# Performance work log

Measured on AMD Instinct MI355X. Metric: run time of the kernel, lower is better.

The kernel has to match this reference:

```python
import jax, jax.numpy as jnp
import numpy as np

B, C, L = 16, 256, 2048

def setup_inputs() -> dict:
    key = jax.random.key(0)
    y = jax.random.normal(key, (B, C, L), dtype=jnp.float32)
    alpha = jnp.float32(0.5)
    beta = jnp.float32(0.5)
    gamma = jnp.float32(0.0)
    return {"y": y, "alpha": alpha, "beta": beta, "gamma": gamma}

def reference(y, alpha, beta, gamma):
    # y: [B, C, L]
    Bs, Cs, Ls = y.shape
    # channel attention: scores over channels, scaled by 1/sqrt(L)
    scale_c = 1.0 / np.sqrt(max(Ls, 1)).astype(np.float32)
    scores_c = jnp.einsum('bcl,bdl->bcd', y, y) * scale_c          # [B, C, C]
    attn_c = jax.nn.softmax(scores_c, axis=-1)
    y_c = jnp.einsum('bcd,bdl->bcl', attn_c, y)                    # [B, C, L]
    # time attention: scores over time steps, scaled by 1/sqrt(C)
    scale_t = 1.0 / np.sqrt(max(Cs, 1)).astype(np.float32)
    scores_t = jnp.einsum('bcl,bcm->blm', y, y) * scale_t          # [B, L, L]
    attn_t = jax.nn.softmax(scores_t, axis=-1)
    y_t = jnp.einsum('blm,bcm->bcl', attn_t, y)                    # [B, C, L]
    # learnable weighted combine + residual (gamma)
    out = alpha * y_c + beta * y_t + gamma * y
    return out
```

## Files before the change

### kernel.cpp

```cpp
#include <hip/hip_runtime.h>

#define B_ 16
#define C_ 256
#define L_ 2048

typedef __attribute__((ext_vector_type(8))) short short8;
typedef __attribute__((ext_vector_type(4))) float float4v;

__device__ inline float4v mfma16(short8 a, short8 b, float4v c) {
  return __builtin_amdgcn_mfma_f32_16x16x32_bf16(a, b, c, 0, 0, 0);
}

__device__ inline ushort f2bf(float x) {
  union { float f; unsigned u; } v; v.f = x;
  unsigned r = (v.u + 0x7fffu + ((v.u >> 16) & 1u)) >> 16;
  return (ushort)r;
}

__device__ inline void dma16(const ushort* g, void* l) {
  __builtin_amdgcn_global_load_lds(
      (const __attribute__((address_space(1))) unsigned int*)(g),
      (__attribute__((address_space(3))) unsigned int*)(l), 16, 0, 0);
}

#define BAR_FULL() asm volatile("s_waitcnt vmcnt(0) lgkmcnt(0)\ns_barrier" ::: "memory")
#define BAR_LGKM() asm volatile("s_waitcnt lgkmcnt(0)\ns_barrier" ::: "memory")

__global__ __launch_bounds__(256) void cvt_kernel(const float* __restrict__ y,
                                                  ushort* __restrict__ yb,
                                                  ushort* __restrict__ ytb) {
  __shared__ float tile[32][33];
  int b = blockIdx.z, ct = blockIdx.y, lt = blockIdx.x;
  int tx = threadIdx.x & 31, ty = threadIdx.x >> 5;
  size_t base = ((size_t)b * C_ + (size_t)ct * 32) * L_ + (size_t)lt * 32;
#pragma unroll
  for (int i = 0; i < 4; ++i) {
    int r = ty + i * 8;
    float v = y[base + (size_t)r * L_ + tx];
    tile[r][tx] = v;
    yb[base + (size_t)r * L_ + tx] = f2bf(v);
  }
  __syncthreads();
  size_t tbase = ((size_t)b * L_ + (size_t)lt * 32) * C_ + (size_t)ct * 32;
#pragma unroll
  for (int i = 0; i < 4; ++i) {
    int r = ty + i * 8;
    ytb[tbase + (size_t)r * C_ + tx] = f2bf(tile[tx][r]);
  }
}

__global__ __launch_bounds__(256) void chan_kernel(
    const ushort* __restrict__ yb, const ushort* __restrict__ ytb,
    const float* __restrict__ y, float* __restrict__ out,
    const float* __restrict__ alpha_p, const float* __restrict__ gamma_p) {
  const int blk = blockIdx.x;
  const int b = (blk & 7) + 8 * ((blk >> 3) & 1);
  const int rest = blk >> 4;
  const int m0 = (rest & 15) * 16;
  const int Lh = rest >> 4;
  const int tid = threadIdx.x;
  const int w = tid >> 6, lane = tid & 63, quad = lane >> 4, l16 = lane & 15;
  const float scale = 0.022097086912079608f;
  const float SHIFT = 45.0f;

  __shared__ __align__(16) unsigned char Tb[2][32768];
  __shared__ ushort Pl[16 * 264];
  __shared__ float wsum[4][16];
  __shared__ float ginvb[16];

  const ushort* Yb = yb + (size_t)b * C_ * L_;
  const ushort* Yt = ytb + (size_t)b * L_ * C_;
  const int chq = ((lane & 3) - ((lane >> 3) & 3)) & 3;
  const int sK = (quad + ((l16 >> 1) & 3)) & 3;
  const int frag_lane = l16 * 64 + sK * 16;

  const ushort* ap[8];
#pragma unroll
  for (int j = 0; j < 8; ++j) {
    int gi = w * 8 + j, kk2 = gi >> 4, chgrp = gi & 15;
    ap[j] = Yb + (size_t)chgrp * 16 * L_ + kk2 * 32 + (lane >> 2) * L_ + chq * 8;
  }
  const ushort* vp[8];
#pragma unroll
  for (int j = 0; j < 8; ++j) {
    int gi = w * 8 + j, pg = gi >> 3, kk = gi & 7;
    vp[j] = Yt + (size_t)(Lh * 1024 + pg * 16 + (lane >> 2)) * C_ + kk * 32 + chq * 8;
  }

#pragma unroll
  for (int j = 0; j < 8; ++j) {
    dma16(ap[j], (void*)(Tb[0] + (w * 8 + j) * 1024));
    ap[j] += 64;
  }

  float4v acc[4];
#pragma unroll
  for (int nt = 0; nt < 4; ++nt) acc[nt] = (float4v){0.f, 0.f, 0.f, 0.f};

  for (int c = 0; c < 32; ++c) {
    BAR_FULL();
    if (c < 31) {
      unsigned char* bp = Tb[(c + 1) & 1];
#pragma unroll
      for (int j = 0; j < 8; ++j) {
        dma16(ap[j], (void*)(bp + (w * 8 + j) * 1024));
        ap[j] += 64;
      }
    } else {
#pragma unroll
      for (int j = 0; j < 8; ++j) {
        dma16(vp[j], (void*)(Tb[0] + (w * 8 + j) * 1024));
        vp[j] += (size_t)64 * C_;
      }
    }
    const unsigned char* cbuf = Tb[c & 1];
#pragma unroll
    for (int kk2 = 0; kk2 < 2; ++kk2) {
      short8 aA = *(const short8*)(cbuf + (kk2 * 16 + (m0 >> 4)) * 1024 + frag_lane);
#pragma unroll
      for (int nt = 0; nt < 4; ++nt) {
        short8 bB = *(const short8*)(cbuf + (kk2 * 16 + w * 4 + nt) * 1024 + frag_lane);
        acc[nt] = mfma16(aA, bB, acc[nt]);
      }
    }
  }

  float rs[4] = {0.f, 0.f, 0.f, 0.f};
#pragma unroll
  for (int nt = 0; nt < 4; ++nt)
#pragma unroll
    for (int r = 0; r < 4; ++r) {
      float p = __expf(fmaf(acc[nt][r], scale, -SHIFT));
      rs[r] += p;
      Pl[(quad * 4 + r) * 264 + w * 64 + nt * 16 + l16] = f2bf(p);
    }
#pragma unroll
  for (int r = 0; r < 4; ++r)
#pragma unroll
    for (int off = 1; off < 16; off <<= 1) rs[r] += __shfl_xor(rs[r], off);
  if (l16 == 0) {
#pragma unroll
    for (int r = 0; r < 4; ++r) wsum[w][quad * 4 + r] = rs[r];
  }
  __syncthreads();
  if (tid < 16)
    ginvb[tid] = 1.0f / (wsum[0][tid] + wsum[1][tid] + wsum[2][tid] + wsum[3][tid]);
  __syncthreads();

  const float alpha = alpha_p[0], gamma = gamma_p[0];
  short8 Af[8];
#pragma unroll
  for (int ks = 0; ks < 8; ++ks)
    Af[ks] = *(const short8*)(&Pl[l16 * 264 + ks * 32 + quad * 8]);
  float gvr[4];
#pragma unroll
  for (int r = 0; r < 4; ++r) gvr[r] = alpha * ginvb[quad * 4 + r];

  for (int cb = 0; cb < 16; ++cb) {
    BAR_FULL();
    if (cb < 15) {
      unsigned char* bp = Tb[(cb + 1) & 1];
#pragma unroll
      for (int j = 0; j < 8; ++j) {
        dma16(vp[j], (void*)(bp + (w * 8 + j) * 1024));
        vp[j] += (size_t)64 * C_;
      }
    }
    const unsigned char* vb = Tb[cb & 1];
    float4v f = (float4v){0.f, 0.f, 0.f, 0.f};
#pragma unroll
    for (int kk = 0; kk < 8; ++kk) {
      short8 bf = *(const short8*)(vb + (w * 8 + kk) * 1024 + frag_lane);
      f = mfma16(Af[kk], bf, f);
    }
    int col = Lh * 1024 + cb * 64 + w * 16 + l16;
#pragma unroll
    for (int r = 0; r < 4; ++r) {
      int row = m0 + quad * 4 + r;
      size_t idx = ((size_t)b * C_ + row) * L_ + col;
      out[idx] = fmaf(gvr[r], f[r], gamma * y[idx]);
    }
  }
}

__global__ __launch_bounds__(256, 2) void time_kernel(
    const ushort* __restrict__ yb, const ushort* __restrict__ ytb,
    float* __restrict__ out, const float* __restrict__ beta_p) {
  const int blk = blockIdx.x;
  const int b = (blk & 7) + 8 * ((blk >> 3) & 1);
  const int m0 = (blk >> 4) * 64;
  const int tid = threadIdx.x;
  const int w = tid >> 6, lane = tid & 63, quad = lane >> 4, l16 = lane & 15;
  const int mtw = w >> 1, kt2 = w & 1;
  const float scale = 0.0625f;
  const float SHIFT = 16.0f;

  __shared__ __align__(16) unsigned char buf[2][32768];
  __shared__ ushort Pd[64 * 40];
  __shared__ float wsum[4][64];
  __shared__ float ginv[64];

  const ushort* Yt = ytb + (size_t)b * L_ * C_;
  const ushort* Yb = yb + (size_t)b * C_ * L_;
  const int chq = ((lane & 3) - ((lane >> 3) & 3)) & 3;
  const int klK = (lane >> 2) * C_ + chq * 8;
  const int vlV = (lane >> 2) * L_ + chq * 8;
  const int sK = (quad + ((l16 >> 1) & 3)) & 3;
  const int frag_lane = l16 * 64 + sK * 16;

  short8 Qf[2][8];
#pragma unroll
  for (int mt = 0; mt < 2; ++mt)
#pragma unroll
    for (int kk = 0; kk < 8; ++kk)
      Qf[mt][kk] = *(const short8*)(Yt + (size_t)(m0 + mtw * 32 + mt * 16 + l16) * C_ +
                                    kk * 32 + quad * 8);

  const ushort* dp[8];
#pragma unroll
  for (int j = 0; j < 8; ++j) {
    int gi = w * 8 + j;
    if (gi < 16) {
      int kk = gi >> 1, g = gi & 1;
      dp[j] = Yt + (size_t)(g * 16) * C_ + kk * 32 + klK;
    } else {
      int cg = gi - 16;
      dp[j] = Yb + (size_t)cg * 16 * L_ + vlV;
    }
  }
  const int dstride = (w < 2) ? 32 * C_ : 32;

  float4v facc[4][4];
#pragma unroll
  for (int mt = 0; mt < 4; ++mt)
#pragma unroll
    for (int nt = 0; nt < 4; ++nt) facc[mt][nt] = (float4v){0.f, 0.f, 0.f, 0.f};
  float rs[2][4] = {{0.f, 0.f, 0.f, 0.f}, {0.f, 0.f, 0.f, 0.f}};

#pragma unroll
  for (int j = 0; j < 8; ++j) {
    dma16(dp[j], (void*)(buf[0] + (w * 8 + j) * 1024));
    dp[j] += dstride;
  }

  for (int c = 0; c < 64; ++c) {
    const int cb = c & 1;
    BAR_FULL();
    if (c < 63) {
      unsigned char* bp = buf[cb ^ 1];
#pragma unroll
      for (int j = 0; j < 8; ++j) {
        dma16(dp[j], (void*)(bp + (w * 8 + j) * 1024));
        dp[j] += dstride;
      }
    }
    float4v s0 = (float4v){0.f, 0.f, 0.f, 0.f};
    float4v s1 = (float4v){0.f, 0.f, 0.f, 0.f};
#pragma unroll
    for (int kk = 0; kk < 8; ++kk) {
      short8 bf = *(const short8*)(buf[cb] + (kk * 2 + kt2) * 1024 + frag_lane);
      s0 = mfma16(Qf[0][kk], bf, s0);
      s1 = mfma16(Qf[1][kk], bf, s1);
    }
#pragma unroll
    for (int mt = 0; mt < 2; ++mt) {
      float4v s = mt ? s1 : s0;
#pragma unroll
      for (int r = 0; r < 4; ++r) {
        float p = __expf(fmaf(s[r], scale, -SHIFT));
        rs[mt][r] += p;
        Pd[(mtw * 32 + mt * 16 + quad * 4 + r) * 40 + kt2 * 16 + l16] = f2bf(p);
      }
    }
    BAR_LGKM();
#pragma unroll
    for (int mt = 0; mt < 4; ++mt) {
      short8 va = *(const short8*)(buf[cb] + (16 + w * 4 + mt) * 1024 + frag_lane);
#pragma unroll
      for (int nt = 0; nt < 4; ++nt) {
        short8 pb = *(const short8*)(&Pd[(nt * 16 + l16) * 40 + quad * 8]);
        facc[mt][nt] = mfma16(va, pb, facc[mt][nt]);
      }
    }
  }

  __syncthreads();
#pragma unroll
  for (int mt = 0; mt < 2; ++mt)
#pragma unroll
    for (int r = 0; r < 4; ++r)
#pragma unroll
      for (int off = 1; off < 16; off <<= 1) rs[mt][r] += __shfl_xor(rs[mt][r], off);
  if (l16 == 0) {
#pragma unroll
    for (int mt = 0; mt < 2; ++mt)
#pragma unroll
      for (int r = 0; r < 4; ++r)
        wsum[w][mtw * 32 + mt * 16 + quad * 4 + r] = rs[mt][r];
  }
  __syncthreads();
  if (tid < 64) {
    int mh = tid >> 5;
    ginv[tid] = 1.0f / (wsum[mh * 2][tid] + wsum[mh * 2 + 1][tid]);
  }
  __syncthreads();

  const float beta = beta_p[0];
  float gq[4];
#pragma unroll
  for (int nt = 0; nt < 4; ++nt) gq[nt] = beta * ginv[nt * 16 + l16];

#pragma unroll
  for (int mt = 0; mt < 4; ++mt)
#pragma unroll
    for (int nt = 0; nt < 4; ++nt)
#pragma unroll
      for (int r = 0; r < 4; ++r) {
        int ch = w * 64 + mt * 16 + quad * 4 + r;
        size_t idx = ((size_t)b * C_ + ch) * L_ + m0 + nt * 16 + l16;
        out[idx] = fmaf(gq[nt], facc[mt][nt][r], out[idx]);
      }
}

extern "C" void kernel_launch(void* const* d_in, const int* in_sizes, int n_in,
                              void* d_out, int out_size, void* d_ws, size_t ws_size,
                              hipStream_t stream) {
  const float* y = (const float*)d_in[0];
  const float* alpha = (const float*)d_in[1];
  const float* beta = (const float*)d_in[2];
  const float* gamma = (const float*)d_in[3];
  float* out = (float*)d_out;

  ushort* yb = (ushort*)d_ws;
  ushort* ytb = yb + (size_t)B_ * C_ * L_;

  hipLaunchKernelGGL(cvt_kernel, dim3(L_ / 32, C_ / 32, B_), dim3(256), 0, stream,
                     y, yb, ytb);
  hipLaunchKernelGGL(chan_kernel, dim3(512), dim3(256), 0, stream,
                     yb, ytb, y, out, alpha, gamma);
  hipLaunchKernelGGL(time_kernel, dim3(512), dim3(256), 0, stream,
                     yb, ytb, out, beta);
}
```

Before: 232.6 us.

## Replace LDS DMA staging with direct register-prefetched global loads in attention kernels

Both the channel and time attention kernels stop staging K/V tiles through double-buffered shared memory filled by global_load_lds DMA. Each wave now loads its MFMA fragments straight from global memory into registers, double-buffered one step ahead. The time kernel double-buffers the P tile in LDS so one barrier per step suffices, and chan_kernel gets an occupancy hint of 3 blocks per SU. The goal is to cut LDS traffic and barriers, at the cost of redundant global/L2 reads across waves, less coalesced loads, and higher register pressure.

Result: slower. 435.0 us (+87.0%).

```diff
diff --git a/kernel.cpp b/kernel.cpp
--- a/kernel.cpp
+++ b/kernel.cpp
@@ -17,13 +17,6 @@
   return (ushort)r;
 }
 
-__device__ inline void dma16(const ushort* g, void* l) {
-  __builtin_amdgcn_global_load_lds(
-      (const __attribute__((address_space(1))) unsigned int*)(g),
-      (__attribute__((address_space(3))) unsigned int*)(l), 16, 0, 0);
-}
-
-#define BAR_FULL() asm volatile("s_waitcnt vmcnt(0) lgkmcnt(0)\ns_barrier" ::: "memory")
 #define BAR_LGKM() asm volatile("s_waitcnt lgkmcnt(0)\ns_barrier" ::: "memory")
 
 __global__ __launch_bounds__(256) void cvt_kernel(const float* __restrict__ y,
@@ -49,7 +42,7 @@
   }
 }
 
-__global__ __launch_bounds__(256) void chan_kernel(
+__global__ __launch_bounds__(256, 3) void chan_kernel(
     const ushort* __restrict__ yb, const ushort* __restrict__ ytb,
     const float* __restrict__ y, float* __restrict__ out,
     const float* __restrict__ alpha_p, const float* __restrict__ gamma_p) {
@@ -63,66 +56,39 @@
   const float scale = 0.022097086912079608f;
   const float SHIFT = 45.0f;
 
-  __shared__ __align__(16) unsigned char Tb[2][32768];
   __shared__ ushort Pl[16 * 264];
   __shared__ float wsum[4][16];
   __shared__ float ginvb[16];
 
   const ushort* Yb = yb + (size_t)b * C_ * L_;
   const ushort* Yt = ytb + (size_t)b * L_ * C_;
-  const int chq = ((lane & 3) - ((lane >> 3) & 3)) & 3;
-  const int sK = (quad + ((l16 >> 1) & 3)) & 3;
-  const int frag_lane = l16 * 64 + sK * 16;
-
-  const ushort* ap[8];
-#pragma unroll
-  for (int j = 0; j < 8; ++j) {
-    int gi = w * 8 + j, kk2 = gi >> 4, chgrp = gi & 15;
-    ap[j] = Yb + (size_t)chgrp * 16 * L_ + kk2 * 32 + (lane >> 2) * L_ + chq * 8;
-  }
-  const ushort* vp[8];
-#pragma unroll
-  for (int j = 0; j < 8; ++j) {
-    int gi = w * 8 + j, pg = gi >> 3, kk = gi & 7;
-    vp[j] = Yt + (size_t)(Lh * 1024 + pg * 16 + (lane >> 2)) * C_ + kk * 32 + chq * 8;
-  }
-
-#pragma unroll
-  for (int j = 0; j < 8; ++j) {
-    dma16(ap[j], (void*)(Tb[0] + (w * 8 + j) * 1024));
-    ap[j] += 64;
-  }
+
+  const ushort* arow = Yb + (size_t)(m0 + l16) * L_ + quad * 8;
+  const ushort* brow[4];
+#pragma unroll
+  for (int nt = 0; nt < 4; ++nt)
+    brow[nt] = Yb + (size_t)((w * 4 + nt) * 16 + l16) * L_ + quad * 8;
 
   float4v acc[4];
 #pragma unroll
   for (int nt = 0; nt < 4; ++nt) acc[nt] = (float4v){0.f, 0.f, 0.f, 0.f};
 
-  for (int c = 0; c < 32; ++c) {
-    BAR_FULL();
-    if (c < 31) {
-      unsigned char* bp = Tb[(c + 1) & 1];
-#pragma unroll
-      for (int j = 0; j < 8; ++j) {
-        dma16(ap[j], (void*)(bp + (w * 8 + j) * 1024));
-        ap[j] += 64;
-      }
-    } else {
-#pragma unroll
-      for (int j = 0; j < 8; ++j) {
-        dma16(vp[j], (void*)(Tb[0] + (w * 8 + j) * 1024));
-        vp[j] += (size_t)64 * C_;
-      }
-    }
-    const unsigned char* cbuf = Tb[c & 1];
-#pragma unroll
-    for (int kk2 = 0; kk2 < 2; ++kk2) {
-      short8 aA = *(const short8*)(cbuf + (kk2 * 16 + (m0 >> 4)) * 1024 + frag_lane);
-#pragma unroll
-      for (int nt = 0; nt < 4; ++nt) {
-        short8 bB = *(const short8*)(cbuf + (kk2 * 16 + w * 4 + nt) * 1024 + frag_lane);
-        acc[nt] = mfma16(aA, bB, acc[nt]);
-      }
-    }
+  short8 ab[2], bb[2][4];
+  ab[0] = *(const short8*)(arow);
+#pragma unroll
+  for (int nt = 0; nt < 4; ++nt) bb[0][nt] = *(const short8*)(brow[nt]);
+
+#pragma unroll 2
+  for (int kk = 0; kk < 64; ++kk) {
+    const int t = kk & 1;
+    if (kk < 63) {
+      int ko = (kk + 1) * 32;
+      ab[t ^ 1] = *(const short8*)(arow + ko);
+#pragma unroll
+      for (int nt = 0; nt < 4; ++nt) bb[t ^ 1][nt] = *(const short8*)(brow[nt] + ko);
+    }
+#pragma unroll
+    for (int nt = 0; nt < 4; ++nt) acc[nt] = mfma16(ab[t], bb[t][nt], acc[nt]);
   }
 
   float rs[4] = {0.f, 0.f, 0.f, 0.f};
@@ -142,10 +108,10 @@
 #pragma unroll
     for (int r = 0; r < 4; ++r) wsum[w][quad * 4 + r] = rs[r];
   }
-  __syncthreads();
+  BAR_LGKM();
   if (tid < 16)
     ginvb[tid] = 1.0f / (wsum[0][tid] + wsum[1][tid] + wsum[2][tid] + wsum[3][tid]);
-  __syncthreads();
+  BAR_LGKM();
 
   const float alpha = alpha_p[0], gamma = gamma_p[0];
   short8 Af[8];
@@ -156,24 +122,25 @@
 #pragma unroll
   for (int r = 0; r < 4; ++r) gvr[r] = alpha * ginvb[quad * 4 + r];
 
-  for (int cb = 0; cb < 16; ++cb) {
-    BAR_FULL();
-    if (cb < 15) {
-      unsigned char* bp = Tb[(cb + 1) & 1];
-#pragma unroll
-      for (int j = 0; j < 8; ++j) {
-        dma16(vp[j], (void*)(bp + (w * 8 + j) * 1024));
-        vp[j] += (size_t)64 * C_;
-      }
-    }
-    const unsigned char* vb = Tb[cb & 1];
+  const int nbase = Lh * 1024 + w * 256;
+  short8 vbB[2][8];
+#pragma unroll
+  for (int kk = 0; kk < 8; ++kk)
+    vbB[0][kk] = *(const short8*)(Yt + (size_t)(nbase + l16) * C_ + kk * 32 + quad * 8);
+
+#pragma unroll 2
+  for (int s = 0; s < 16; ++s) {
+    const int t = s & 1;
+    if (s < 15) {
+      int n1 = nbase + (s + 1) * 16;
+#pragma unroll
+      for (int kk = 0; kk < 8; ++kk)
+        vbB[t ^ 1][kk] = *(const short8*)(Yt + (size_t)(n1 + l16) * C_ + kk * 32 + quad * 8);
+    }
     float4v f = (float4v){0.f, 0.f, 0.f, 0.f};
 #pragma unroll
-    for (int kk = 0; kk < 8; ++kk) {
-      short8 bf = *(const short8*)(vb + (w * 8 + kk) * 1024 + frag_lane);
-      f = mfma16(Af[kk], bf, f);
-    }
-    int col = Lh * 1024 + cb * 64 + w * 16 + l16;
+    for (int kk = 0; kk < 8; ++kk) f = mfma16(Af[kk], vbB[t][kk], f);
+    int col = nbase + s * 16 + l16;
 #pragma unroll
     for (int r = 0; r < 4; ++r) {
       int row = m0 + quad * 4 + r;
@@ -195,18 +162,12 @@
   const float scale = 0.0625f;
   const float SHIFT = 16.0f;
 
-  __shared__ __align__(16) unsigned char buf[2][32768];
-  __shared__ ushort Pd[64 * 40];
+  __shared__ ushort Pd[2][64 * 40];
   __shared__ float wsum[4][64];
   __shared__ float ginv[64];
 
   const ushort* Yt = ytb + (size_t)b * L_ * C_;
   const ushort* Yb = yb + (size_t)b * C_ * L_;
-  const int chq = ((lane & 3) - ((lane >> 3) & 3)) & 3;
-  const int klK = (lane >> 2) * C_ + chq * 8;
-  const int vlV = (lane >> 2) * L_ + chq * 8;
-  const int sK = (quad + ((l16 >> 1) & 3)) & 3;
-  const int frag_lane = l16 * 64 + sK * 16;
 
   short8 Qf[2][8];
 #pragma unroll
@@ -216,19 +177,11 @@
       Qf[mt][kk] = *(const short8*)(Yt + (size_t)(m0 + mtw * 32 + mt * 16 + l16) * C_ +
                                     kk * 32 + quad * 8);
 
-  const ushort* dp[8];
-#pragma unroll
-  for (int j = 0; j < 8; ++j) {
-    int gi = w * 8 + j;
-    if (gi < 16) {
-      int kk = gi >> 1, g = gi & 1;
-      dp[j] = Yt + (size_t)(g * 16) * C_ + kk * 32 + klK;
-    } else {
-      int cg = gi - 16;
-      dp[j] = Yb + (size_t)cg * 16 * L_ + vlV;
-    }
-  }
-  const int dstride = (w < 2) ? 32 * C_ : 32;
+  const ushort* krp = Yt + (size_t)(kt2 * 16 + l16) * C_ + quad * 8;
+  const ushort* vrp[4];
+#pragma unroll
+  for (int mt = 0; mt < 4; ++mt)
+    vrp[mt] = Yb + (size_t)(w * 64 + mt * 16 + l16) * L_ + quad * 8;
 
   float4v facc[4][4];
 #pragma unroll
@@ -237,30 +190,29 @@
     for (int nt = 0; nt < 4; ++nt) facc[mt][nt] = (float4v){0.f, 0.f, 0.f, 0.f};
   float rs[2][4] = {{0.f, 0.f, 0.f, 0.f}, {0.f, 0.f, 0.f, 0.f}};
 
-#pragma unroll
-  for (int j = 0; j < 8; ++j) {
-    dma16(dp[j], (void*)(buf[0] + (w * 8 + j) * 1024));
-    dp[j] += dstride;
-  }
-
+  short8 kb[2][8];
+#pragma unroll
+  for (int kk = 0; kk < 8; ++kk) kb[0][kk] = *(const short8*)(krp + kk * 32);
+
+#pragma unroll 2
   for (int c = 0; c < 64; ++c) {
     const int cb = c & 1;
-    BAR_FULL();
+    const int kc = c * 32;
     if (c < 63) {
-      unsigned char* bp = buf[cb ^ 1];
-#pragma unroll
-      for (int j = 0; j < 8; ++j) {
-        dma16(dp[j], (void*)(bp + (w * 8 + j) * 1024));
-        dp[j] += dstride;
-      }
-    }
+      const ushort* kp1 = krp + (size_t)(kc + 32) * C_;
+#pragma unroll
+      for (int kk = 0; kk < 8; ++kk) kb[cb ^ 1][kk] = *(const short8*)(kp1 + kk * 32);
+    }
+    short8 vb[4];
+#pragma unroll
+    for (int mt = 0; mt < 4; ++mt) vb[mt] = *(const short8*)(vrp[mt] + kc);
+
     float4v s0 = (float4v){0.f, 0.f, 0.f, 0.f};
     float4v s1 = (float4v){0.f, 0.f, 0.f, 0.f};
 #pragma unroll
     for (int kk = 0; kk < 8; ++kk) {
-      short8 bf = *(const short8*)(buf[cb] + (kk * 2 + kt2) * 1024 + frag_lane);
-      s0 = mfma16(Qf[0][kk], bf, s0);
-      s1 = mfma16(Qf[1][kk], bf, s1);
+      s0 = mfma16(Qf[0][kk], kb[cb][kk], s0);
+      s1 = mfma16(Qf[1][kk], kb[cb][kk], s1);
     }
 #pragma unroll
     for (int mt = 0; mt < 2; ++mt) {
@@ -269,19 +221,19 @@
       for (int r = 0; r < 4; ++r) {
         float p = __expf(fmaf(s[r], scale, -SHIFT));
         rs[mt][r] += p;
-        Pd[(mtw * 32 + mt * 16 + quad * 4 + r) * 40 + kt2 * 16 + l16] = f2bf(p);
+        Pd[cb][(mtw * 32 + mt * 16 + quad * 4 + r) * 40 + kt2 * 16 + l16] = f2bf(p);
       }
     }
     BAR_LGKM();
-#pragma unroll
-    for (int mt = 0; mt < 4; ++mt) {
-      short8 va = *(const short8*)(buf[cb] + (16 + w * 4 + mt) * 1024 + frag_lane);
-#pragma unroll
-      for (int nt = 0; nt < 4; ++nt) {
-        short8 pb = *(const short8*)(&Pd[(nt * 16 + l16) * 40 + quad * 8]);
-        facc[mt][nt] = mfma16(va, pb, facc[mt][nt]);
-      }
-    }
+    short8 pb[4];
+#pragma unroll
+    for (int nt = 0; nt < 4; ++nt)
+      pb[nt] = *(const short8*)(&Pd[cb][(nt * 16 + l16) * 40 + quad * 8]);
+#pragma unroll
+    for (int mt = 0; mt < 4; ++mt)
+#pragma unroll
+      for (int nt = 0; nt < 4; ++nt)
+        facc[mt][nt] = mfma16(vb[mt], pb[nt], facc[mt][nt]);
   }
 
   __syncthreads();
```

## Split channel softmax to global P and fuse channel PV into time kernel

Applied to the files above, without the earlier changes.

The channel-attention probabilities and their row normalisers are now computed once per 16 rows into a workspace, instead of once per L-half as before. The channel P·V product is folded into the time-attention kernel, which combines both results and writes the output once. This removes the separate read-modify-write pass over the output and the duplicated score computation. The cost is extra MFMA work, register pressure in the time kernel, and a workspace round trip for P. The gamma residual now reads the bf16 copy of y and is skipped entirely when gamma is zero, which changes precision slightly.

Result: faster. 217.1 us (-6.6%).

```diff
diff --git a/kernel.cpp b/kernel.cpp
--- a/kernel.cpp
+++ b/kernel.cpp
@@ -15,6 +15,11 @@
   union { float f; unsigned u; } v; v.f = x;
   unsigned r = (v.u + 0x7fffu + ((v.u >> 16) & 1u)) >> 16;
   return (ushort)r;
+}
+
+__device__ inline float bf2f(ushort u) {
+  union { unsigned u; float f; } v; v.u = ((unsigned)u) << 16;
+  return v.f;
 }
 
 __device__ inline void dma16(const ushort* g, void* l) {
@@ -49,68 +54,45 @@
   }
 }
 
-__global__ __launch_bounds__(256) void chan_kernel(
-    const ushort* __restrict__ yb, const ushort* __restrict__ ytb,
-    const float* __restrict__ y, float* __restrict__ out,
-    const float* __restrict__ alpha_p, const float* __restrict__ gamma_p) {
+__global__ __launch_bounds__(256) void pk_kernel(const ushort* __restrict__ yb,
+                                                 ushort* __restrict__ Pc,
+                                                 float* __restrict__ ginvC) {
   const int blk = blockIdx.x;
   const int b = (blk & 7) + 8 * ((blk >> 3) & 1);
-  const int rest = blk >> 4;
-  const int m0 = (rest & 15) * 16;
-  const int Lh = rest >> 4;
+  const int m0 = (blk >> 4) * 16;
   const int tid = threadIdx.x;
   const int w = tid >> 6, lane = tid & 63, quad = lane >> 4, l16 = lane & 15;
   const float scale = 0.022097086912079608f;
   const float SHIFT = 45.0f;
 
   __shared__ __align__(16) unsigned char Tb[2][32768];
-  __shared__ ushort Pl[16 * 264];
   __shared__ float wsum[4][16];
-  __shared__ float ginvb[16];
 
   const ushort* Yb = yb + (size_t)b * C_ * L_;
-  const ushort* Yt = ytb + (size_t)b * L_ * C_;
   const int chq = ((lane & 3) - ((lane >> 3) & 3)) & 3;
+  const int dl = (lane >> 2) * L_ + chq * 8;
   const int sK = (quad + ((l16 >> 1) & 3)) & 3;
   const int frag_lane = l16 * 64 + sK * 16;
 
-  const ushort* ap[8];
+  float4v acc[4];
+#pragma unroll
+  for (int nt = 0; nt < 4; ++nt) acc[nt] = (float4v){0.f, 0.f, 0.f, 0.f};
+
 #pragma unroll
   for (int j = 0; j < 8; ++j) {
     int gi = w * 8 + j, kk2 = gi >> 4, chgrp = gi & 15;
-    ap[j] = Yb + (size_t)chgrp * 16 * L_ + kk2 * 32 + (lane >> 2) * L_ + chq * 8;
-  }
-  const ushort* vp[8];
-#pragma unroll
-  for (int j = 0; j < 8; ++j) {
-    int gi = w * 8 + j, pg = gi >> 3, kk = gi & 7;
-    vp[j] = Yt + (size_t)(Lh * 1024 + pg * 16 + (lane >> 2)) * C_ + kk * 32 + chq * 8;
-  }
-
-#pragma unroll
-  for (int j = 0; j < 8; ++j) {
-    dma16(ap[j], (void*)(Tb[0] + (w * 8 + j) * 1024));
-    ap[j] += 64;
-  }
-
-  float4v acc[4];
-#pragma unroll
-  for (int nt = 0; nt < 4; ++nt) acc[nt] = (float4v){0.f, 0.f, 0.f, 0.f};
+    dma16(Yb + (size_t)chgrp * 16 * L_ + kk2 * 32 + dl, (void*)(Tb[0] + gi * 1024));
+  }
 
   for (int c = 0; c < 32; ++c) {
     BAR_FULL();
     if (c < 31) {
+      int kc = (c + 1) * 64;
       unsigned char* bp = Tb[(c + 1) & 1];
 #pragma unroll
       for (int j = 0; j < 8; ++j) {
-        dma16(ap[j], (void*)(bp + (w * 8 + j) * 1024));
-        ap[j] += 64;
-      }
-    } else {
-#pragma unroll
-      for (int j = 0; j < 8; ++j) {
-        dma16(vp[j], (void*)(Tb[0] + (w * 8 + j) * 1024));
-        vp[j] += (size_t)64 * C_;
+        int gi = w * 8 + j, kk2 = gi >> 4, chgrp = gi & 15;
+        dma16(Yb + (size_t)chgrp * 16 * L_ + kc + kk2 * 32 + dl, (void*)(bp + gi * 1024));
       }
     }
     const unsigned char* cbuf = Tb[c & 1];
@@ -125,15 +107,20 @@
     }
   }
 
-  float rs[4] = {0.f, 0.f, 0.f, 0.f};
+  float p[4][4], rs[4] = {0.f, 0.f, 0.f, 0.f};
 #pragma unroll
   for (int nt = 0; nt < 4; ++nt)
 #pragma unroll
     for (int r = 0; r < 4; ++r) {
-      float p = __expf(fmaf(acc[nt][r], scale, -SHIFT));
-      rs[r] += p;
-      Pl[(quad * 4 + r) * 264 + w * 64 + nt * 16 + l16] = f2bf(p);
-    }
+      p[nt][r] = __expf(fmaf(acc[nt][r], scale, -SHIFT));
+      rs[r] += p[nt][r];
+    }
+  ushort* Pb = Pc + ((size_t)b * 256 + m0) * 256;
+#pragma unroll
+  for (int nt = 0; nt < 4; ++nt)
+#pragma unroll
+    for (int r = 0; r < 4; ++r)
+      Pb[(quad * 4 + r) * 256 + w * 64 + nt * 16 + l16] = f2bf(p[nt][r]);
 #pragma unroll
   for (int r = 0; r < 4; ++r)
 #pragma unroll
@@ -144,48 +131,15 @@
   }
   __syncthreads();
   if (tid < 16)
-    ginvb[tid] = 1.0f / (wsum[0][tid] + wsum[1][tid] + wsum[2][tid] + wsum[3][tid]);
-  __syncthreads();
-
-  const float alpha = alpha_p[0], gamma = gamma_p[0];
-  short8 Af[8];
-#pragma unroll
-  for (int ks = 0; ks < 8; ++ks)
-    Af[ks] = *(const short8*)(&Pl[l16 * 264 + ks * 32 + quad * 8]);
-  float gvr[4];
-#pragma unroll
-  for (int r = 0; r < 4; ++r) gvr[r] = alpha * ginvb[quad * 4 + r];
-
-  for (int cb = 0; cb < 16; ++cb) {
-    BAR_FULL();
-    if (cb < 15) {
-      unsigned char* bp = Tb[(cb + 1) & 1];
-#pragma unroll
-      for (int j = 0; j < 8; ++j) {
-        dma16(vp[j], (void*)(bp + (w * 8 + j) * 1024));
-        vp[j] += (size_t)64 * C_;
-      }
-    }
-    const unsigned char* vb = Tb[cb & 1];
-    float4v f = (float4v){0.f, 0.f, 0.f, 0.f};
-#pragma unroll
-    for (int kk = 0; kk < 8; ++kk) {
-      short8 bf = *(const short8*)(vb + (w * 8 + kk) * 1024 + frag_lane);
-      f = mfma16(Af[kk], bf, f);
-    }
-    int col = Lh * 1024 + cb * 64 + w * 16 + l16;
-#pragma unroll
-    for (int r = 0; r < 4; ++r) {
-      int row = m0 + quad * 4 + r;
-      size_t idx = ((size_t)b * C_ + row) * L_ + col;
-      out[idx] = fmaf(gvr[r], f[r], gamma * y[idx]);
-    }
-  }
-}
-
-__global__ __launch_bounds__(256, 2) void time_kernel(
+    ginvC[b * 256 + m0 + tid] =
+        1.0f / (wsum[0][tid] + wsum[1][tid] + wsum[2][tid] + wsum[3][tid]);
+}
+
+__global__ __launch_bounds__(256, 2) void ct_kernel(
     const ushort* __restrict__ yb, const ushort* __restrict__ ytb,
-    float* __restrict__ out, const float* __restrict__ beta_p) {
+    const ushort* __restrict__ Pc, const float* __restrict__ ginvC,
+    float* __restrict__ out, const float* __restrict__ alpha_p,
+    const float* __restrict__ beta_p, const float* __restrict__ gamma_p) {
   const int blk = blockIdx.x;
   const int b = (blk & 7) + 8 * ((blk >> 3) & 1);
   const int m0 = (blk >> 4) * 64;
@@ -202,9 +156,11 @@
 
   const ushort* Yt = ytb + (size_t)b * L_ * C_;
   const ushort* Yb = yb + (size_t)b * C_ * L_;
+  const ushort* Pcb = Pc + (size_t)b * 256 * 256;
   const int chq = ((lane & 3) - ((lane >> 3) & 3)) & 3;
   const int klK = (lane >> 2) * C_ + chq * 8;
   const int vlV = (lane >> 2) * L_ + chq * 8;
+  const int pcl = (lane >> 2) * 256 + chq * 8;
   const int sK = (quad + ((l16 >> 1) & 3)) & 3;
   const int frag_lane = l16 * 64 + sK * 16;
 
@@ -215,6 +171,51 @@
     for (int kk = 0; kk < 8; ++kk)
       Qf[mt][kk] = *(const short8*)(Yt + (size_t)(m0 + mtw * 32 + mt * 16 + l16) * C_ +
                                     kk * 32 + quad * 8);
+  const ushort* qgrow[2];
+#pragma unroll
+  for (int mt = 0; mt < 2; ++mt)
+    qgrow[mt] = Yt + (size_t)(m0 + (1 - mtw) * 32 + mt * 16 + l16) * C_ + quad * 8;
+
+  float4v fc[4][4];
+#pragma unroll
+  for (int mt = 0; mt < 4; ++mt)
+#pragma unroll
+    for (int nt = 0; nt < 4; ++nt) fc[mt][nt] = (float4v){0.f, 0.f, 0.f, 0.f};
+
+  short8 qg[2][2];
+#pragma unroll
+  for (int mt = 0; mt < 2; ++mt) qg[0][mt] = *(const short8*)(qgrow[mt]);
+#pragma unroll
+  for (int j = 0; j < 4; ++j) {
+    int gi = w * 4 + j;
+    dma16(Pcb + (size_t)(gi * 16) * 256 + pcl, (void*)(buf[0] + gi * 1024));
+  }
+
+  for (int c2 = 0; c2 < 8; ++c2) {
+    const int cb = c2 & 1;
+    BAR_FULL();
+    if (c2 < 7) {
+      unsigned char* bp = buf[cb ^ 1];
+#pragma unroll
+      for (int j = 0; j < 4; ++j) {
+        int gi = w * 4 + j;
+        dma16(Pcb + (size_t)(gi * 16) * 256 + (c2 + 1) * 32 + pcl,
+              (void*)(bp + gi * 1024));
+      }
+#pragma unroll
+      for (int mt = 0; mt < 2; ++mt)
+        qg[cb ^ 1][mt] = *(const short8*)(qgrow[mt] + (c2 + 1) * 32);
+    }
+#pragma unroll
+    for (int mt = 0; mt < 4; ++mt) {
+      short8 Ac = *(const short8*)(buf[cb] + (w * 4 + mt) * 1024 + frag_lane);
+#pragma unroll
+      for (int nt = 0; nt < 4; ++nt) {
+        short8 Bq = ((nt >> 1) == mtw) ? Qf[nt & 1][c2] : qg[cb][nt & 1];
+        fc[mt][nt] = mfma16(Ac, Bq, fc[mt][nt]);
+      }
+    }
+  }
 
   const ushort* dp[8];
 #pragma unroll
@@ -230,11 +231,11 @@
   }
   const int dstride = (w < 2) ? 32 * C_ : 32;
 
-  float4v facc[4][4];
+  float4v ft[4][4];
 #pragma unroll
   for (int mt = 0; mt < 4; ++mt)
 #pragma unroll
-    for (int nt = 0; nt < 4; ++nt) facc[mt][nt] = (float4v){0.f, 0.f, 0.f, 0.f};
+    for (int nt = 0; nt < 4; ++nt) ft[mt][nt] = (float4v){0.f, 0.f, 0.f, 0.f};
   float rs[2][4] = {{0.f, 0.f, 0.f, 0.f}, {0.f, 0.f, 0.f, 0.f}};
 
 #pragma unroll
@@ -279,7 +280,7 @@
 #pragma unroll
       for (int nt = 0; nt < 4; ++nt) {
         short8 pb = *(const short8*)(&Pd[(nt * 16 + l16) * 40 + quad * 8]);
-        facc[mt][nt] = mfma16(va, pb, facc[mt][nt]);
+        ft[mt][nt] = mfma16(va, pb, ft[mt][nt]);
       }
     }
   }
@@ -305,21 +306,41 @@
   }
   __syncthreads();
 
-  const float beta = beta_p[0];
+  const float alpha = alpha_p[0], beta = beta_p[0], gamma = gamma_p[0];
   float gq[4];
 #pragma unroll
   for (int nt = 0; nt < 4; ++nt) gq[nt] = beta * ginv[nt * 16 + l16];
-
+  float gc[4][4];
 #pragma unroll
   for (int mt = 0; mt < 4; ++mt)
 #pragma unroll
-    for (int nt = 0; nt < 4; ++nt)
-#pragma unroll
-      for (int r = 0; r < 4; ++r) {
-        int ch = w * 64 + mt * 16 + quad * 4 + r;
-        size_t idx = ((size_t)b * C_ + ch) * L_ + m0 + nt * 16 + l16;
-        out[idx] = fmaf(gq[nt], facc[mt][nt][r], out[idx]);
-      }
+    for (int r = 0; r < 4; ++r)
+      gc[mt][r] = alpha * ginvC[b * 256 + w * 64 + mt * 16 + quad * 4 + r];
+
+  if (gamma != 0.0f) {
+#pragma unroll
+    for (int mt = 0; mt < 4; ++mt)
+#pragma unroll
+      for (int nt = 0; nt < 4; ++nt)
+#pragma unroll
+        for (int r = 0; r < 4; ++r) {
+          int ch = w * 64 + mt * 16 + quad * 4 + r;
+          size_t idx = ((size_t)b * C_ + ch) * L_ + m0 + nt * 16 + l16;
+          float v = gc[mt][r] * fc[mt][nt][r] + gq[nt] * ft[mt][nt][r];
+          out[idx] = fmaf(gamma, bf2f(Yb[(size_t)ch * L_ + m0 + nt * 16 + l16]), v);
+        }
+  } else {
+#pragma unroll
+    for (int mt = 0; mt < 4; ++mt)
+#pragma unroll
+      for (int nt = 0; nt < 4; ++nt)
+#pragma unroll
+        for (int r = 0; r < 4; ++r) {
+          int ch = w * 64 + mt * 16 + quad * 4 + r;
+          size_t idx = ((size_t)b * C_ + ch) * L_ + m0 + nt * 16 + l16;
+          out[idx] = gc[mt][r] * fc[mt][nt][r] + gq[nt] * ft[mt][nt][r];
+        }
+  }
 }
 
 extern "C" void kernel_launch(void* const* d_in, const int* in_sizes, int n_in,
@@ -333,11 +354,12 @@
 
   ushort* yb = (ushort*)d_ws;
   ushort* ytb = yb + (size_t)B_ * C_ * L_;
+  ushort* Pc = ytb + (size_t)B_ * C_ * L_;
+  float* ginvC = (float*)(Pc + (size_t)B_ * 256 * 256);
 
   hipLaunchKernelGGL(cvt_kernel, dim3(L_ / 32, C_ / 32, B_), dim3(256), 0, stream,
                      y, yb, ytb);
-  hipLaunchKernelGGL(chan_kernel, dim3(512), dim3(256), 0, stream,
-                     yb, ytb, y, out, alpha, gamma);
-  hipLaunchKernelGGL(time_kernel, dim3(512), dim3(256), 0, stream,
-                     yb, ytb, out, beta);
-}
+  hipLaunchKernelGGL(pk_kernel, dim3(256), dim3(256), 0, stream, yb, Pc, ginvC);
+  hipLaunchKernelGGL(ct_kernel, dim3(512), dim3(256), 0, stream,
+                     yb, ytb, Pc, ginvC, out, alpha, beta, gamma);
+}
```
